# Optimization experiments

Measured on AMD Instinct MI355X. Metric: run time of the kernel, lower is better.

## Reference

```python
import jax, jax.numpy as jnp
import numpy as np

NFEAT, NHID = 128, 128

def setup_inputs() -> dict:
    key = jax.random.key(0)
    k1, k2, k3, k4 = jax.random.split(key, 4)
    x = jax.random.normal(k1, (32, 1024, NFEAT), dtype=jnp.float32)
    adj = jax.random.uniform(k2, (32, 1024, 1024), dtype=jnp.float32)
    # GraphConvolution parameters (Kipf init ~ uniform, scale irrelevant for correctness)
    bound = 1.0 / np.sqrt(NHID)
    W = jax.random.uniform(k3, (NFEAT, NHID), dtype=jnp.float32, minval=-bound, maxval=bound)
    b = jax.random.uniform(k4, (NHID,), dtype=jnp.float32, minval=-bound, maxval=bound)
    return {"x": x, "adj": adj, "W": W, "b": b}

def reference(x, adj, W, b):
    # Batched equivalent of the per-sample python loop:
    # out[i] = relu(adj[i] @ (x[i] @ W) + b); dropout is identity in eval mode.
    support = jnp.einsum('bnf,fh->bnh', x, W)          # [B, N, nhid]
    out = jnp.einsum('bnm,bmh->bnh', adj, support) + b  # [B, N, nhid]
    return jax.nn.relu(out)
```

## Files before the change

kernel.cpp:

```cpp
#include <hip/hip_runtime.h>
#include <hip/hip_bf16.h>
#include <stdint.h>


typedef short bf16x8 __attribute__((ext_vector_type(8)));
typedef float f32x4 __attribute__((ext_vector_type(4)));
typedef int i32x4 __attribute__((ext_vector_type(4)));
typedef unsigned short u16x4 __attribute__((ext_vector_type(4)));

__device__ __forceinline__ unsigned short f2bf(float f) {
    uint32_t u = __builtin_bit_cast(uint32_t, f);
    u += 0x7FFFu + ((u >> 16) & 1u);
    return (unsigned short)(u >> 16);
}

__device__ __forceinline__ bf16x8 cvt8(f32x4 v0, f32x4 v1) {
    union { __hip_bfloat162 h[4]; bf16x8 v; } u;
    u.h[0] = __float22bfloat162_rn(make_float2(v0.x, v0.y));
    u.h[1] = __float22bfloat162_rn(make_float2(v0.z, v0.w));
    u.h[2] = __float22bfloat162_rn(make_float2(v1.x, v1.y));
    u.h[3] = __float22bfloat162_rn(make_float2(v1.z, v1.w));
    return u.v;
}

#define GLOAD_LDS16(g, s)                                         \
    __builtin_amdgcn_global_load_lds(                             \
        (const __attribute__((address_space(1))) void*)(g),       \
        (__attribute__((address_space(3))) void*)(s), 16, 0, 0)

#define K1S 136
__global__ __launch_bounds__(256) void k1_support(const float* __restrict__ x,
                                                  const float* __restrict__ W,
                                                  unsigned short* __restrict__ ST) {
    __shared__ __align__(16) unsigned short xt[64 * K1S];
    __shared__ __align__(16) unsigned short wt[128 * K1S];
    int t = threadIdx.x;
    int node_base = blockIdx.x * 64;

    const f32x4* xg = (const f32x4*)(x + (size_t)node_base * 128);
#pragma unroll
    for (int i = 0; i < 8; ++i) {
        int f4 = i * 256 + t;
        int row = f4 >> 5, c4 = f4 & 31;
        f32x4 v = xg[f4];
        u16x4 p;
        p.x = f2bf(v.x); p.y = f2bf(v.y); p.z = f2bf(v.z); p.w = f2bf(v.w);
        *(u16x4*)&xt[row * K1S + c4 * 4] = p;
    }
#pragma unroll
    for (int i = 0; i < 16; ++i) {
        int c = i * 256 + t;
        int f = c >> 5, h4 = c & 31;
        f32x4 v = *(const f32x4*)(W + f * 128 + h4 * 4);
        wt[(h4 * 4 + 0) * K1S + f] = f2bf(v.x);
        wt[(h4 * 4 + 1) * K1S + f] = f2bf(v.y);
        wt[(h4 * 4 + 2) * K1S + f] = f2bf(v.z);
        wt[(h4 * 4 + 3) * K1S + f] = f2bf(v.w);
    }
    __syncthreads();

    int wv = t >> 6, lane = t & 63, l16 = lane & 15, quad = lane >> 4;
    int wave_h = (wv & 1) * 64, wave_m = (wv >> 1) * 32;

    f32x4 acc[4][2];
#pragma unroll
    for (int ht = 0; ht < 4; ++ht)
#pragma unroll
        for (int mt = 0; mt < 2; ++mt) acc[ht][mt] = 0.f;

#pragma unroll
    for (int s = 0; s < 4; ++s) {
        int ko = s * 32 + quad * 8;
        bf16x8 a[4], bb[2];
#pragma unroll
        for (int ht = 0; ht < 4; ++ht)
            a[ht] = *(const bf16x8*)&wt[(wave_h + ht * 16 + l16) * K1S + ko];
#pragma unroll
        for (int mt = 0; mt < 2; ++mt)
            bb[mt] = *(const bf16x8*)&xt[(wave_m + mt * 16 + l16) * K1S + ko];
#pragma unroll
        for (int ht = 0; ht < 4; ++ht)
#pragma unroll
            for (int mt = 0; mt < 2; ++mt)
                acc[ht][mt] = __builtin_amdgcn_mfma_f32_16x16x32_bf16(
                    a[ht], bb[mt], acc[ht][mt], 0, 0, 0);
    }

    int batch = blockIdx.x >> 4;
    int m_in_b = (blockIdx.x & 15) * 64;
#pragma unroll
    for (int ht = 0; ht < 4; ++ht)
#pragma unroll
        for (int mt = 0; mt < 2; ++mt) {
            int mcol = wave_m + mt * 16 + l16;
#pragma unroll
            for (int r = 0; r < 4; ++r) {
                int h = wave_h + ht * 16 + quad * 4 + r;
                ST[(((size_t)batch * 128 + h) << 10) + m_in_b + mcol] =
                    f2bf(acc[ht][mt][r]);
            }
        }
}

__global__ __launch_bounds__(256) void k2_gcn(const float* __restrict__ adj,
                                              const unsigned short* __restrict__ ST,
                                              const float* __restrict__ bias,
                                              float* __restrict__ out) {
    __shared__ __align__(16) float As[64 * 64];
    __shared__ __align__(16) unsigned short Bs[128 * 64];
    const int t = threadIdx.x;
    const int wv = t >> 6, l = t & 63, l16 = l & 15, quad = l >> 4;
    const int batch = blockIdx.x >> 4;
    const int mbase = (blockIdx.x & 15) * 64;

    const float* adjb = adj + ((size_t)batch * 1024 + mbase) * 1024;
    const unsigned short* stb = ST + ((size_t)batch * 128) * 1024;

    const int cA = l & 15, cB = l & 7;
    const float* gA[4];
    const unsigned short* gB[4];
    float* ldsA[4];
    unsigned short* ldsB[4];
#pragma unroll
    for (int i = 0; i < 4; ++i) {
        int ra = wv * 16 + i * 4 + (l >> 4);
        gA[i] = adjb + (size_t)ra * 1024 + ((cA ^ (2 * (ra & 7))) << 2);
        ldsA[i] = &As[(wv * 16 + i * 4) * 64];
        int rb = wv * 32 + i * 8 + (l >> 3);
        gB[i] = stb + (size_t)rb * 1024 + ((cB ^ (rb & 7)) << 3);
        ldsB[i] = &Bs[(wv * 32 + i * 8) * 64];
    }

    const int wave_m = (wv & 1) * 32, wave_n = (wv >> 1) * 64;
    float bv[4];
#pragma unroll
    for (int j = 0; j < 4; ++j) bv[j] = bias[wave_n + j * 16 + l16];

    f32x4 acc[2][4];
#pragma unroll
    for (int i = 0; i < 2; ++i)
#pragma unroll
        for (int j = 0; j < 4; ++j) acc[i][j] = 0.f;

    for (int kb = 0; kb < 16; ++kb) {
#pragma unroll
        for (int i = 0; i < 4; ++i) {
            GLOAD_LDS16(gA[i] + kb * 64, ldsA[i]);
            GLOAD_LDS16(gB[i] + kb * 64, ldsB[i]);
        }
        __syncthreads();
#pragma unroll
        for (int s = 0; s < 2; ++s) {
            bf16x8 a[2], bb[4];
#pragma unroll
            for (int i = 0; i < 2; ++i) {
                int ra = wave_m + i * 16 + l16;
                int pp = (((s * 4 + quad) ^ (ra & 7)) << 3);
                f32x4 v0 = *(const f32x4*)&As[ra * 64 + pp];
                f32x4 v1 = *(const f32x4*)&As[ra * 64 + pp + 4];
                a[i] = cvt8(v0, v1);
            }
#pragma unroll
            for (int j = 0; j < 4; ++j) {
                int nb = wave_n + j * 16 + l16;
                int cc = (((s * 4 + quad) ^ (nb & 7)) << 3);
                bb[j] = *(const bf16x8*)&Bs[nb * 64 + cc];
            }
#pragma unroll
            for (int i = 0; i < 2; ++i)
#pragma unroll
                for (int j = 0; j < 4; ++j)
                    acc[i][j] = __builtin_amdgcn_mfma_f32_16x16x32_bf16(
                        a[i], bb[j], acc[i][j], 0, 0, 0);
        }
        __syncthreads();
    }

    float* outb = out + ((size_t)batch * 1024 + mbase) * 128;
#pragma unroll
    for (int i = 0; i < 2; ++i)
#pragma unroll
        for (int j = 0; j < 4; ++j) {
            int n = wave_n + j * 16 + l16;
#pragma unroll
            for (int r = 0; r < 4; ++r) {
                int m = wave_m + i * 16 + quad * 4 + r;
                float v = acc[i][j][r] + bv[j];
                outb[(size_t)m * 128 + n] = fmaxf(v, 0.f);
            }
        }
}

extern "C" void kernel_launch(void* const* d_in, const int* in_sizes, int n_in,
                              void* d_out, int out_size, void* d_ws, size_t ws_size,
                              hipStream_t stream) {
    const float* x = (const float*)d_in[0];
    const float* adj = (const float*)d_in[1];
    const float* W = (const float*)d_in[2];
    const float* b = (const float*)d_in[3];
    float* out = (float*)d_out;

    unsigned short* ST = (unsigned short*)d_ws;

    k1_support<<<512, 256, 0, stream>>>(x, W, ST);
    k2_gcn<<<512, 256, 0, stream>>>(adj, ST, b, out);
}
```

Baseline: 229.7 us.

## Load GEMM operands directly from global memory into registers, drop LDS staging

The aggregation kernel no longer stages adj and support tiles through shared memory with global_load_lds and barriers. Each lane now loads its MFMA fragments straight from global memory and converts adj to bf16 in registers, with the K loop unrolled by four. This removes the LDS traffic and the __syncthreads calls. In exchange, the two waves that share rows re-read the same adj and support data from global memory and rely on L2 to absorb it, and each lane's 32-byte strided row accesses may coalesce less well.

```diff
diff --git a/kernel.cpp b/kernel.cpp
--- a/kernel.cpp
+++ b/kernel.cpp
@@ -5,7 +5,6 @@
 
 typedef short bf16x8 __attribute__((ext_vector_type(8)));
 typedef float f32x4 __attribute__((ext_vector_type(4)));
-typedef int i32x4 __attribute__((ext_vector_type(4)));
 typedef unsigned short u16x4 __attribute__((ext_vector_type(4)));
 
 __device__ __forceinline__ unsigned short f2bf(float f) {
@@ -22,11 +21,6 @@
     u.h[3] = __float22bfloat162_rn(make_float2(v1.z, v1.w));
     return u.v;
 }
-
-#define GLOAD_LDS16(g, s)                                         \
-    __builtin_amdgcn_global_load_lds(                             \
-        (const __attribute__((address_space(1))) void*)(g),       \
-        (__attribute__((address_space(3))) void*)(s), 16, 0, 0)
 
 #define K1S 136
 __global__ __launch_bounds__(256) void k1_support(const float* __restrict__ x,
@@ -106,32 +100,23 @@
                                               const unsigned short* __restrict__ ST,
                                               const float* __restrict__ bias,
                                               float* __restrict__ out) {
-    __shared__ __align__(16) float As[64 * 64];
-    __shared__ __align__(16) unsigned short Bs[128 * 64];
     const int t = threadIdx.x;
     const int wv = t >> 6, l = t & 63, l16 = l & 15, quad = l >> 4;
     const int batch = blockIdx.x >> 4;
     const int mbase = (blockIdx.x & 15) * 64;
+    const int wave_m = (wv & 1) * 32, wave_n = (wv >> 1) * 64;
 
-    const float* adjb = adj + ((size_t)batch * 1024 + mbase) * 1024;
-    const unsigned short* stb = ST + ((size_t)batch * 128) * 1024;
+    const float* pA[2];
+    const unsigned short* pB[4];
+#pragma unroll
+    for (int i = 0; i < 2; ++i)
+        pA[i] = adj + ((size_t)(batch * 1024 + mbase + wave_m + i * 16 + l16) * 1024
+                       + quad * 8);
+#pragma unroll
+    for (int j = 0; j < 4; ++j)
+        pB[j] = ST + ((size_t)(batch * 128 + wave_n + j * 16 + l16) * 1024
+                      + quad * 8);
 
-    const int cA = l & 15, cB = l & 7;
-    const float* gA[4];
-    const unsigned short* gB[4];
-    float* ldsA[4];
-    unsigned short* ldsB[4];
-#pragma unroll
-    for (int i = 0; i < 4; ++i) {
-        int ra = wv * 16 + i * 4 + (l >> 4);
-        gA[i] = adjb + (size_t)ra * 1024 + ((cA ^ (2 * (ra & 7))) << 2);
-        ldsA[i] = &As[(wv * 16 + i * 4) * 64];
-        int rb = wv * 32 + i * 8 + (l >> 3);
-        gB[i] = stb + (size_t)rb * 1024 + ((cB ^ (rb & 7)) << 3);
-        ldsB[i] = &Bs[(wv * 32 + i * 8) * 64];
-    }
-
-    const int wave_m = (wv & 1) * 32, wave_n = (wv >> 1) * 64;
     float bv[4];
 #pragma unroll
     for (int j = 0; j < 4; ++j) bv[j] = bias[wave_n + j * 16 + l16];
@@ -142,38 +127,24 @@
 #pragma unroll
         for (int j = 0; j < 4; ++j) acc[i][j] = 0.f;
 
-    for (int kb = 0; kb < 16; ++kb) {
+#pragma unroll 4
+    for (int kc = 0; kc < 32; ++kc) {
+        bf16x8 a[2], bb[4];
 #pragma unroll
-        for (int i = 0; i < 4; ++i) {
-            GLOAD_LDS16(gA[i] + kb * 64, ldsA[i]);
-            GLOAD_LDS16(gB[i] + kb * 64, ldsB[i]);
+        for (int i = 0; i < 2; ++i) {
+            f32x4 v0 = *(const f32x4*)(pA[i] + kc * 32);
+            f32x4 v1 = *(const f32x4*)(pA[i] + kc * 32 + 4);
+            a[i] = cvt8(v0, v1);
         }
-        __syncthreads();
 #pragma unroll
-        for (int s = 0; s < 2; ++s) {
-            bf16x8 a[2], bb[4];
+        for (int j = 0; j < 4; ++j)
+            bb[j] = *(const bf16x8*)(pB[j] + kc * 32);
 #pragma unroll
-            for (int i = 0; i < 2; ++i) {
-                int ra = wave_m + i * 16 + l16;
-                int pp = (((s * 4 + quad) ^ (ra & 7)) << 3);
-                f32x4 v0 = *(const f32x4*)&As[ra * 64 + pp];
-                f32x4 v1 = *(const f32x4*)&As[ra * 64 + pp + 4];
-                a[i] = cvt8(v0, v1);
-            }
+        for (int i = 0; i < 2; ++i)
 #pragma unroll
-            for (int j = 0; j < 4; ++j) {
-                int nb = wave_n + j * 16 + l16;
-                int cc = (((s * 4 + quad) ^ (nb & 7)) << 3);
-                bb[j] = *(const bf16x8*)&Bs[nb * 64 + cc];
-            }
-#pragma unroll
-            for (int i = 0; i < 2; ++i)
-#pragma unroll
-                for (int j = 0; j < 4; ++j)
-                    acc[i][j] = __builtin_amdgcn_mfma_f32_16x16x32_bf16(
-                        a[i], bb[j], acc[i][j], 0, 0, 0);
-        }
-        __syncthreads();
+            for (int j = 0; j < 4; ++j)
+                acc[i][j] = __builtin_amdgcn_mfma_f32_16x16x32_bf16(
+                    a[i], bb[j], acc[i][j], 0, 0, 0);
     }
 
     float* outb = out + ((size_t)batch * 1024 + mbase) * 128;
```

After: 253.3 us. 10.2% more time.
